# Performance work log

Hardware: AMD Instinct MI355X
Metric: run time of the kernel (lower is better)

## Reference

```python
import jax, jax.numpy as jnp
import numpy as np

N = 20000   # num_perts (nodes)
E = 640000  # edges
H = 2       # attention heads
D = 64      # hidden_dim = out_dim
L = 4       # num_layers
NEG_SLOPE_ATT = 0.2    # GATv2 attention leaky_relu
NEG_SLOPE_ACT = 0.01   # F.leaky_relu default


def setup_inputs() -> dict:
    key = jax.random.key(0)
    ks = jax.random.split(key, 9)
    s = 0.1
    return {
        "edge_index": jax.random.randint(ks[0], (2, E), 0, N, dtype=jnp.int64 if jax.config.x64_enabled else jnp.int32),
        "edge_weight": jax.random.uniform(ks[1], (E,), jnp.float32),
        "pert_emb": jax.random.normal(ks[2], (N, D), jnp.float32) * s,
        "Wl": jax.random.normal(ks[3], (L, D, H * D), jnp.float32) * s,
        "bl": jnp.zeros((L, H * D), jnp.float32),
        "Wr": jax.random.normal(ks[4], (L, D, H * D), jnp.float32) * s,
        "br": jnp.zeros((L, H * D), jnp.float32),
        "att": jax.random.normal(ks[5], (L, H, D), jnp.float32) * s,
        "bias": jnp.zeros((L, D), jnp.float32),
        "Wo": jax.random.normal(ks[6], (D, D), jnp.float32) * s,
        "bo": jnp.zeros((D,), jnp.float32),
    }


def _gatv2_layer(x, src, dst, Wl, bl, Wr, br, att, bias):
    # x: [N, D] -> out: [N, D] (heads averaged, concat=False)
    xl = (x @ Wl + bl).reshape(N, H, D)  # source transform
    xr = (x @ Wr + br).reshape(N, H, D)  # target transform
    e = jax.nn.leaky_relu(xl[src] + xr[dst], NEG_SLOPE_ATT)        # [E,H,D]
    logits = jnp.einsum('ehd,hd->eh', e, att)                      # [E,H]
    # segment softmax over incoming edges per target node
    m = jax.ops.segment_max(logits, dst, num_segments=N)           # [N,H]
    m = jnp.where(jnp.isfinite(m), m, 0.0)
    ex = jnp.exp(logits - m[dst])
    denom = jax.ops.segment_sum(ex, dst, num_segments=N)           # [N,H]
    alpha = ex / (denom[dst] + 1e-16)                              # [E,H]
    msg = xl[src] * alpha[:, :, None]                              # [E,H,D]
    out = jax.ops.segment_sum(msg, dst, num_segments=N)            # [N,H,D]
    return out.mean(axis=1) + bias                                 # [N,D]


def reference(edge_index, edge_weight, pert_emb, Wl, bl, Wr, br, att, bias, Wo, bo):
    del edge_weight  # use_edge_weight=False -> edge_weight set to None
    src, dst = edge_index[0], edge_index[1]
    x = pert_emb  # embedding lookup of arange(num_perts) == full table
    for i in range(L):
        x = _gatv2_layer(x, src, dst, Wl[i], bl[i], Wr[i], br[i], att[i], bias[i])
        x = jax.nn.leaky_relu(x, NEG_SLOPE_ACT)  # dropout p=0.0 is identity
    x = x @ Wo + bo
    x = jax.nn.leaky_relu(x, NEG_SLOPE_ACT)
    return x
```

## Files before the change

### kernel.cpp

```cpp
#include <hip/hip_runtime.h>
#include <hip/hip_fp16.h>
#include <math.h>
#include <float.h>

#define NN 20000
#define EE 640000
#define HH 2
#define DD 64
#define LL 4
#define HD 128
#define CAP 80
#define GR 32
#define GEMM_BLOCKS (NN / GR)
#define SCAT_BLOCKS ((EE + 255) / 256)
#define NPB 4
#define LOG2E 1.4426950408889634f

typedef _Float16 half4 __attribute__((ext_vector_type(4)));
typedef _Float16 half8 __attribute__((ext_vector_type(8)));

__device__ __forceinline__ half4 f2h(float a, float b, float c, float d) {
    half4 r;
    r.x = (_Float16)a; r.y = (_Float16)b; r.z = (_Float16)c; r.w = (_Float16)d;
    return r;
}

__device__ __forceinline__ float grp8_sum(float x) {
    int t;
    t = __builtin_amdgcn_update_dpp(0, __float_as_int(x), 0xB1, 0xF, 0xF, true);
    x += __int_as_float(t);
    t = __builtin_amdgcn_update_dpp(0, __float_as_int(x), 0x4E, 0xF, 0xF, true);
    x += __int_as_float(t);
    t = __builtin_amdgcn_update_dpp(0, __float_as_int(x), 0x141, 0xF, 0xF, true);
    x += __int_as_float(t);
    return x;
}

__global__ void __launch_bounds__(256) prep_kernel(
        const float* __restrict__ x,
        const float* __restrict__ Wl, const float* __restrict__ bl,
        const float* __restrict__ Wr, const float* __restrict__ br,
        _Float16* __restrict__ xl, _Float16* __restrict__ xr,
        const int* __restrict__ src, const int* __restrict__ dst,
        int* __restrict__ cnt, int* __restrict__ csr_src) {
    int tid = threadIdx.x;
    if (blockIdx.x >= GEMM_BLOCKS) {
        int e = (blockIdx.x - GEMM_BLOCKS) * 256 + tid;
        if (e < EE) {
            int d = dst[e];
            int pos = atomicAdd(&cnt[d], 1);
            if (pos < CAP) csr_src[d * CAP + pos] = src[e];
        }
        return;
    }
    __shared__ float xs[16][GR];
    __shared__ float ws[16][2 * HD];
    int row0 = blockIdx.x * GR;
    int tc = tid & 63;
    int tr = tid >> 6;
    int c0 = tc * 4;

    float4 bv;
    {
        const float* bsrc = (c0 < HD) ? (bl + c0) : (br + (c0 - HD));
        bv = *(const float4*)bsrc;
    }
    float acc[8][4];
#pragma unroll
    for (int r = 0; r < 8; ++r) {
        acc[r][0] = bv.x; acc[r][1] = bv.y; acc[r][2] = bv.z; acc[r][3] = bv.w;
    }

    int sr = tid >> 3;
    int skk = (tid & 7) * 2;

    for (int kc = 0; kc < DD; kc += 16) {
        __syncthreads();
        {
            float2 v = *(const float2*)&x[(size_t)(row0 + sr) * DD + kc + skk];
            xs[skk][sr] = v.x;
            xs[skk + 1][sr] = v.y;
        }
#pragma unroll
        for (int q = 0; q < 4; ++q) {
            int idx = tid + 256 * q;
            int kk = idx >> 6;
            int cc = (idx & 63) * 4;
            const float* srcp = (cc < HD) ? (Wl + (size_t)(kc + kk) * HD + cc)
                                          : (Wr + (size_t)(kc + kk) * HD + (cc - HD));
            *(float4*)&ws[kk][cc] = *(const float4*)srcp;
        }
        __syncthreads();
#pragma unroll
        for (int kk = 0; kk < 16; ++kk) {
            float4 wv = *(const float4*)&ws[kk][c0];
            float xv[8];
            *(float4*)&xv[0] = *(const float4*)&xs[kk][tr * 8];
            *(float4*)&xv[4] = *(const float4*)&xs[kk][tr * 8 + 4];
#pragma unroll
            for (int r = 0; r < 8; ++r) {
                acc[r][0] = fmaf(xv[r], wv.x, acc[r][0]);
                acc[r][1] = fmaf(xv[r], wv.y, acc[r][1]);
                acc[r][2] = fmaf(xv[r], wv.z, acc[r][2]);
                acc[r][3] = fmaf(xv[r], wv.w, acc[r][3]);
            }
        }
    }

    _Float16* ybase = (c0 < HD) ? xl : xr;
    int cw = (c0 < HD) ? c0 : (c0 - HD);
#pragma unroll
    for (int r = 0; r < 8; ++r) {
        int row = row0 + tr * 8 + r;
        *(half4*)&ybase[(size_t)row * HD + cw] =
            f2h(acc[r][0], acc[r][1], acc[r][2], acc[r][3]);
    }
}

template <bool FINAL>
__global__ void __launch_bounds__(256, 4) fused_aggregate(
        const _Float16* __restrict__ xl, const _Float16* __restrict__ xr,
        const float* __restrict__ att, const int* __restrict__ cnt,
        const int* __restrict__ csr_src, const float* __restrict__ bias,
        const float* __restrict__ Wnl, const float* __restrict__ bnl,
        const float* __restrict__ Wnr, const float* __restrict__ bnr,
        const float* __restrict__ Wo, const float* __restrict__ bo,
        _Float16* __restrict__ xlo, _Float16* __restrict__ xro,
        float* __restrict__ out) {
    int tid = threadIdx.x;
    int lane = tid & 63;
    int w = tid >> 6;
    int node = blockIdx.x * NPB + w;
    int g = lane >> 4;
    int hl = lane & 15;
    int eo = hl * 8;

    __shared__ float sh_o[NPB][DD];
    __shared__ float wst[16][2 * HD];
    __shared__ int   sh_idx[NPB][CAP];

    int start = node * CAP;
    int deg = min(cnt[node], CAP);

    if (lane < CAP / 2) {
        *(int2*)&sh_idx[w][lane * 2] = *(const int2*)&csr_src[start + lane * 2];
    }
    if (lane >= deg) sh_idx[w][lane] = 0;
    {
        int t2 = lane + 64;
        if (t2 >= deg && t2 < CAP) sh_idx[w][t2] = 0;
    }

    unsigned nrow = (unsigned)node << 7;
    const _Float16* xl_eo = xl + eo;

    float xr0, xr1, xr2, xr3, xr4, xr5, xr6, xr7;
    float at0, at1, at2, at3, at4, at5, at6, at7;
    {
        half8 xh = *(const half8*)&xr[nrow + eo];
        xr0 = (float)xh[0]; xr1 = (float)xh[1]; xr2 = (float)xh[2]; xr3 = (float)xh[3];
        xr4 = (float)xh[4]; xr5 = (float)xh[5]; xr6 = (float)xh[6]; xr7 = (float)xh[7];
        float4 a0 = *(const float4*)&att[eo];
        float4 a1 = *(const float4*)&att[eo + 4];
        at0 = a0.x * LOG2E; at1 = a0.y * LOG2E; at2 = a0.z * LOG2E; at3 = a0.w * LOG2E;
        at4 = a1.x * LOG2E; at5 = a1.y * LOG2E; at6 = a1.z * LOG2E; at7 = a1.w * LOG2E;
    }

    float s = 0.f;
    float ac0 = 0.f, ac1 = 0.f, ac2 = 0.f, ac3 = 0.f;
    float ac4 = 0.f, ac5 = 0.f, ac6 = 0.f, ac7 = 0.f;

    if (deg > 0) {
        int niter = (deg + 7) >> 3;

#define IDX2(k) (*(const int2*)&sh_idx[w][8 * min((k), CAP / 8 - 1) + 2 * g])

#define GATHER(H0, H1, k)                                                  \
        {                                                                  \
            int2 r_ = IDX2(k);                                             \
            H0 = *(const half8*)&xl_eo[(unsigned)r_.x << 7];               \
            H1 = *(const half8*)&xl_eo[(unsigned)r_.y << 7];               \
        }

#define COMPUTE(H0, H1, k)                                                 \
        {                                                                  \
            float x00 = (float)H0[0], x01 = (float)H0[1];                  \
            float x02 = (float)H0[2], x03 = (float)H0[3];                  \
            float x04 = (float)H0[4], x05 = (float)H0[5];                  \
            float x06 = (float)H0[6], x07 = (float)H0[7];                  \
            float x10 = (float)H1[0], x11 = (float)H1[1];                  \
            float x12 = (float)H1[2], x13 = (float)H1[3];                  \
            float x14 = (float)H1[4], x15 = (float)H1[5];                  \
            float x16 = (float)H1[6], x17 = (float)H1[7];                  \
            float v, t0 = 0.f, t1 = 0.f;                                   \
            v = x00 + xr0; v = fmaxf(v, 0.2f * v); t0 = fmaf(v, at0, t0);  \
            v = x01 + xr1; v = fmaxf(v, 0.2f * v); t0 = fmaf(v, at1, t0);  \
            v = x02 + xr2; v = fmaxf(v, 0.2f * v); t0 = fmaf(v, at2, t0);  \
            v = x03 + xr3; v = fmaxf(v, 0.2f * v); t0 = fmaf(v, at3, t0);  \
            v = x04 + xr4; v = fmaxf(v, 0.2f * v); t0 = fmaf(v, at4, t0);  \
            v = x05 + xr5; v = fmaxf(v, 0.2f * v); t0 = fmaf(v, at5, t0);  \
            v = x06 + xr6; v = fmaxf(v, 0.2f * v); t0 = fmaf(v, at6, t0);  \
            v = x07 + xr7; v = fmaxf(v, 0.2f * v); t0 = fmaf(v, at7, t0);  \
            v = x10 + xr0; v = fmaxf(v, 0.2f * v); t1 = fmaf(v, at0, t1);  \
            v = x11 + xr1; v = fmaxf(v, 0.2f * v); t1 = fmaf(v, at1, t1);  \
            v = x12 + xr2; v = fmaxf(v, 0.2f * v); t1 = fmaf(v, at2, t1);  \
            v = x13 + xr3; v = fmaxf(v, 0.2f * v); t1 = fmaf(v, at3, t1);  \
            v = x14 + xr4; v = fmaxf(v, 0.2f * v); t1 = fmaf(v, at4, t1);  \
            v = x15 + xr5; v = fmaxf(v, 0.2f * v); t1 = fmaf(v, at5, t1);  \
            v = x16 + xr6; v = fmaxf(v, 0.2f * v); t1 = fmaf(v, at6, t1);  \
            v = x17 + xr7; v = fmaxf(v, 0.2f * v); t1 = fmaf(v, at7, t1);  \
            t0 = grp8_sum(t0);                                             \
            t1 = grp8_sum(t1);                                             \
            int sl_ = 8 * (k) + 2 * g;                                     \
            float w0 = (sl_ < deg) ? exp2f(t0) : 0.f;                      \
            float w1 = (sl_ + 1 < deg) ? exp2f(t1) : 0.f;                  \
            s += w0 + w1;                                                  \
            ac0 = fmaf(w0, x00, fmaf(w1, x10, ac0));                       \
            ac1 = fmaf(w0, x01, fmaf(w1, x11, ac1));                       \
            ac2 = fmaf(w0, x02, fmaf(w1, x12, ac2));                       \
            ac3 = fmaf(w0, x03, fmaf(w1, x13, ac3));                       \
            ac4 = fmaf(w0, x04, fmaf(w1, x14, ac4));                       \
            ac5 = fmaf(w0, x05, fmaf(w1, x15, ac5));                       \
            ac6 = fmaf(w0, x06, fmaf(w1, x16, ac6));                       \
            ac7 = fmaf(w0, x07, fmaf(w1, x17, ac7));                       \
        }

        half8 A0, A1, B0, B1, C0, C1, D0, D1;

        GATHER(A0, A1, 0);
        GATHER(B0, B1, 1);
        GATHER(C0, C1, 2);

        int it = 0;
        while (true) {
            {
                GATHER(D0, D1, it + 3);
                __builtin_amdgcn_sched_barrier(0);
                COMPUTE(A0, A1, it);
            }
            if (++it == niter) break;
            {
                GATHER(A0, A1, it + 3);
                __builtin_amdgcn_sched_barrier(0);
                COMPUTE(B0, B1, it);
            }
            if (++it == niter) break;
            {
                GATHER(B0, B1, it + 3);
                __builtin_amdgcn_sched_barrier(0);
                COMPUTE(C0, C1, it);
            }
            if (++it == niter) break;
            {
                GATHER(C0, C1, it + 3);
                __builtin_amdgcn_sched_barrier(0);
                COMPUTE(D0, D1, it);
            }
            if (++it == niter) break;
        }
#undef IDX2
#undef GATHER
#undef COMPUTE
    }

#pragma unroll
    for (int off = 16; off <= 32; off <<= 1) {
        s   += __shfl_xor(s, off);
        ac0 += __shfl_xor(ac0, off);
        ac1 += __shfl_xor(ac1, off);
        ac2 += __shfl_xor(ac2, off);
        ac3 += __shfl_xor(ac3, off);
        ac4 += __shfl_xor(ac4, off);
        ac5 += __shfl_xor(ac5, off);
        ac6 += __shfl_xor(ac6, off);
        ac7 += __shfl_xor(ac7, off);
    }

    float so  = __shfl_xor(s, 8);
    float ot0 = __shfl_xor(ac0, 8);
    float ot1 = __shfl_xor(ac1, 8);
    float ot2 = __shfl_xor(ac2, 8);
    float ot3 = __shfl_xor(ac3, 8);
    float ot4 = __shfl_xor(ac4, 8);
    float ot5 = __shfl_xor(ac5, 8);
    float ot6 = __shfl_xor(ac6, 8);
    float ot7 = __shfl_xor(ac7, 8);

    if (lane < 8) {
        float inv0 = 1.0f / (s + 1e-16f);
        float inv1 = 1.0f / (so + 1e-16f);
        float4 bv0 = *(const float4*)&bias[lane * 8];
        float4 bv1 = *(const float4*)&bias[lane * 8 + 4];
        float o0 = fmaf(0.5f, fmaf(ac0, inv0, ot0 * inv1), bv0.x);
        float o1 = fmaf(0.5f, fmaf(ac1, inv0, ot1 * inv1), bv0.y);
        float o2 = fmaf(0.5f, fmaf(ac2, inv0, ot2 * inv1), bv0.z);
        float o3 = fmaf(0.5f, fmaf(ac3, inv0, ot3 * inv1), bv0.w);
        float o4 = fmaf(0.5f, fmaf(ac4, inv0, ot4 * inv1), bv1.x);
        float o5 = fmaf(0.5f, fmaf(ac5, inv0, ot5 * inv1), bv1.y);
        float o6 = fmaf(0.5f, fmaf(ac6, inv0, ot6 * inv1), bv1.z);
        float o7 = fmaf(0.5f, fmaf(ac7, inv0, ot7 * inv1), bv1.w);
        o0 = o0 > 0.f ? o0 : 0.01f * o0;
        o1 = o1 > 0.f ? o1 : 0.01f * o1;
        o2 = o2 > 0.f ? o2 : 0.01f * o2;
        o3 = o3 > 0.f ? o3 : 0.01f * o3;
        o4 = o4 > 0.f ? o4 : 0.01f * o4;
        o5 = o5 > 0.f ? o5 : 0.01f * o5;
        o6 = o6 > 0.f ? o6 : 0.01f * o6;
        o7 = o7 > 0.f ? o7 : 0.01f * o7;
        *(float4*)&sh_o[w][lane * 8]     = make_float4(o0, o1, o2, o3);
        *(float4*)&sh_o[w][lane * 8 + 4] = make_float4(o4, o5, o6, o7);
    }

    if (FINAL) {
        float* wlin = &wst[0][0];
        {
            int idx = tid * 16;
            *(float4*)&wlin[idx]      = *(const float4*)&Wo[idx];
            *(float4*)&wlin[idx + 4]  = *(const float4*)&Wo[idx + 4];
            *(float4*)&wlin[idx + 8]  = *(const float4*)&Wo[idx + 8];
            *(float4*)&wlin[idx + 12] = *(const float4*)&Wo[idx + 12];
        }
        __syncthreads();
        int j = lane;
        float og = bo[j];
#pragma unroll 8
        for (int k = 0; k < DD; ++k) {
            og = fmaf(sh_o[w][k], wlin[k * DD + j], og);
        }
        og = og > 0.f ? og : 0.01f * og;
        out[(size_t)node * DD + j] = og;
    } else {
        int c0 = lane * 4;
        float4 acc4;
        {
            const float* bsrc = (c0 < HD) ? (bnl + c0) : (bnr + (c0 - HD));
            acc4 = *(const float4*)bsrc;
        }
        for (int kc = 0; kc < DD; kc += 16) {
            __syncthreads();
#pragma unroll
            for (int q = 0; q < 4; ++q) {
                int idx = tid + 256 * q;
                int kk = idx >> 6;
                int cc = (idx & 63) * 4;
                const float* p = (cc < HD) ? (Wnl + (size_t)(kc + kk) * HD + cc)
                                           : (Wnr + (size_t)(kc + kk) * HD + (cc - HD));
                *(float4*)&wst[kk][cc] = *(const float4*)p;
            }
            __syncthreads();
#pragma unroll
            for (int kk = 0; kk < 16; ++kk) {
                float xo = sh_o[w][kc + kk];
                float4 wv = *(const float4*)&wst[kk][c0];
                acc4.x = fmaf(xo, wv.x, acc4.x);
                acc4.y = fmaf(xo, wv.y, acc4.y);
                acc4.z = fmaf(xo, wv.z, acc4.z);
                acc4.w = fmaf(xo, wv.w, acc4.w);
            }
        }
        half4 hv = f2h(acc4.x, acc4.y, acc4.z, acc4.w);
        if (c0 < HD) *(half4*)&xlo[(size_t)node * HD + c0] = hv;
        else         *(half4*)&xro[(size_t)node * HD + (c0 - HD)] = hv;
    }
}

extern "C" void kernel_launch(void* const* d_in, const int* in_sizes, int n_in,
                              void* d_out, int out_size, void* d_ws, size_t ws_size,
                              hipStream_t stream) {
    const int* edge_index = (const int*)d_in[0];
    const int* src = edge_index;
    const int* dst = edge_index + EE;
    const float* pert = (const float*)d_in[2];
    const float* Wl = (const float*)d_in[3];
    const float* bl = (const float*)d_in[4];
    const float* Wr = (const float*)d_in[5];
    const float* br = (const float*)d_in[6];
    const float* att = (const float*)d_in[7];
    const float* bias = (const float*)d_in[8];
    const float* Wo = (const float*)d_in[9];
    const float* bo = (const float*)d_in[10];
    float* out = (float*)d_out;

    char* w = (char*)d_ws;
    _Float16* xlA = (_Float16*)w;     w += (size_t)NN * HD * 2;
    _Float16* xrA = (_Float16*)w;     w += (size_t)NN * HD * 2;
    _Float16* xlB = (_Float16*)w;     w += (size_t)NN * HD * 2;
    _Float16* xrB = (_Float16*)w;     w += (size_t)NN * HD * 2;
    int* cnt = (int*)w;               w += (size_t)NN * 4;
    int* csr_src = (int*)w;           w += (size_t)NN * CAP * 4;

    hipMemsetAsync(cnt, 0, (size_t)NN * 4, stream);
    prep_kernel<<<GEMM_BLOCKS + SCAT_BLOCKS, 256, 0, stream>>>(
        pert, Wl, bl, Wr, br, xlA, xrA, src, dst, cnt, csr_src);

    _Float16* xls[2] = {xlA, xlB};
    _Float16* xrs[2] = {xrA, xrB};
    for (int l = 0; l < LL - 1; ++l) {
        fused_aggregate<false><<<NN / NPB, 256, 0, stream>>>(
            xls[l & 1], xrs[l & 1], att + (size_t)l * HD, cnt, csr_src,
            bias + (size_t)l * DD,
            Wl + (size_t)(l + 1) * DD * HD, bl + (size_t)(l + 1) * HD,
            Wr + (size_t)(l + 1) * DD * HD, br + (size_t)(l + 1) * HD,
            nullptr, nullptr,
            xls[(l + 1) & 1], xrs[(l + 1) & 1], nullptr);
    }
    fused_aggregate<true><<<NN / NPB, 256, 0, stream>>>(
        xls[(LL - 1) & 1], xrs[(LL - 1) & 1], att + (size_t)(LL - 1) * HD, cnt, csr_src,
        bias + (size_t)(LL - 1) * DD,
        nullptr, nullptr, nullptr, nullptr,
        Wo, bo, nullptr, nullptr, out);
}
```

Baseline: 270.0 us.

## Precompute fp16 transposed next-layer weights and use fdot2 for fused projection

Adds extra prep blocks that convert the next-layer Wl/Wr to fp16, transposed column-major with an 8-element k grouping. The aggregate kernel then loads the whole 256x64 fp16 weight into padded LDS in one go, replacing four float tiles and their barrier pairs. It computes the projection with packed fp16 dot-product instructions. This cuts LDS traffic, barriers and FMA count in the per-node GEMV, at the cost of fp16 activations and weights in the projection, plus a larger LDS footprint (about 36KB) that may lower occupancy.

After: 261.2 us (median of 2 runs). 3.3% less time.

```diff
diff --git a/kernel.cpp b/kernel.cpp
--- a/kernel.cpp
+++ b/kernel.cpp
@@ -13,11 +13,21 @@
 #define GR 32
 #define GEMM_BLOCKS (NN / GR)
 #define SCAT_BLOCKS ((EE + 255) / 256)
+#define WCVT_BLOCKS 24
 #define NPB 4
 #define LOG2E 1.4426950408889634f
-
+#define PADK 72
+
+typedef _Float16 hh2 __attribute__((ext_vector_type(2)));
 typedef _Float16 half4 __attribute__((ext_vector_type(4)));
 typedef _Float16 half8 __attribute__((ext_vector_type(8)));
+
+#if __has_builtin(__builtin_amdgcn_fdot2)
+#define FDOT2(a, b, c) __builtin_amdgcn_fdot2((a), (b), (c), false)
+#else
+#define FDOT2(a, b, c) fmaf((float)(a)[0], (float)(b)[0], \
+                        fmaf((float)(a)[1], (float)(b)[1], (c)))
+#endif
 
 __device__ __forceinline__ half4 f2h(float a, float b, float c, float d) {
     half4 r;
@@ -42,8 +52,31 @@
         const float* __restrict__ Wr, const float* __restrict__ br,
         _Float16* __restrict__ xl, _Float16* __restrict__ xr,
         const int* __restrict__ src, const int* __restrict__ dst,
-        int* __restrict__ cnt, int* __restrict__ csr_src) {
+        int* __restrict__ cnt, int* __restrict__ csr_src,
+        _Float16* __restrict__ wt16) {
     int tid = threadIdx.x;
+    if (blockIdx.x >= GEMM_BLOCKS + SCAT_BLOCKS) {
+        int q = (blockIdx.x - GEMM_BLOCKS - SCAT_BLOCKS) * 256 + tid;
+        int l = q >> 11;
+        int r = q & 2047;
+        int col = r >> 3;
+        int kb = r & 7;
+        const float* base = (col < HD)
+            ? (Wl + (size_t)(l + 1) * DD * HD + col)
+            : (Wr + (size_t)(l + 1) * DD * HD + (col - HD));
+        base += (size_t)(kb * 8) * HD;
+        half8 h;
+        h[0] = (_Float16)base[0 * HD];
+        h[1] = (_Float16)base[1 * HD];
+        h[2] = (_Float16)base[2 * HD];
+        h[3] = (_Float16)base[3 * HD];
+        h[4] = (_Float16)base[4 * HD];
+        h[5] = (_Float16)base[5 * HD];
+        h[6] = (_Float16)base[6 * HD];
+        h[7] = (_Float16)base[7 * HD];
+        *(half8*)&wt16[(size_t)l * 16384 + (size_t)r * 8] = h;
+        return;
+    }
     if (blockIdx.x >= GEMM_BLOCKS) {
         int e = (blockIdx.x - GEMM_BLOCKS) * 256 + tid;
         if (e < EE) {
@@ -122,8 +155,8 @@
         const _Float16* __restrict__ xl, const _Float16* __restrict__ xr,
         const float* __restrict__ att, const int* __restrict__ cnt,
         const int* __restrict__ csr_src, const float* __restrict__ bias,
-        const float* __restrict__ Wnl, const float* __restrict__ bnl,
-        const float* __restrict__ Wnr, const float* __restrict__ bnr,
+        const _Float16* __restrict__ wtn, const float* __restrict__ bnl,
+        const float* __restrict__ bnr,
         const float* __restrict__ Wo, const float* __restrict__ bo,
         _Float16* __restrict__ xlo, _Float16* __restrict__ xro,
         float* __restrict__ out) {
@@ -135,9 +168,9 @@
     int hl = lane & 15;
     int eo = hl * 8;
 
-    __shared__ float sh_o[NPB][DD];
-    __shared__ float wst[16][2 * HD];
-    __shared__ int   sh_idx[NPB][CAP];
+    __shared__ float    sh_o[NPB][DD];
+    __shared__ _Float16 sh_o16[NPB][DD];
+    __shared__ int      sh_idx[NPB][CAP];
 
     int start = node * CAP;
     int deg = min(cnt[node], CAP);
@@ -263,6 +296,9 @@
 #undef COMPUTE
     }
 
+    asm volatile("" ::: "memory");
+    __builtin_amdgcn_sched_barrier(0);
+
 #pragma unroll
     for (int off = 16; off <= 32; off <<= 1) {
         s   += __shfl_xor(s, off);
@@ -307,12 +343,21 @@
         o5 = o5 > 0.f ? o5 : 0.01f * o5;
         o6 = o6 > 0.f ? o6 : 0.01f * o6;
         o7 = o7 > 0.f ? o7 : 0.01f * o7;
-        *(float4*)&sh_o[w][lane * 8]     = make_float4(o0, o1, o2, o3);
-        *(float4*)&sh_o[w][lane * 8 + 4] = make_float4(o4, o5, o6, o7);
+        if (FINAL) {
+            *(float4*)&sh_o[w][lane * 8]     = make_float4(o0, o1, o2, o3);
+            *(float4*)&sh_o[w][lane * 8 + 4] = make_float4(o4, o5, o6, o7);
+        } else {
+            half8 h;
+            h[0] = (_Float16)o0; h[1] = (_Float16)o1;
+            h[2] = (_Float16)o2; h[3] = (_Float16)o3;
+            h[4] = (_Float16)o4; h[5] = (_Float16)o5;
+            h[6] = (_Float16)o6; h[7] = (_Float16)o7;
+            *(half8*)&sh_o16[w][lane * 8] = h;
+        }
     }
 
     if (FINAL) {
-        float* wlin = &wst[0][0];
+        __shared__ float wlin[DD * DD];
         {
             int idx = tid * 16;
             *(float4*)&wlin[idx]      = *(const float4*)&Wo[idx];
@@ -330,37 +375,63 @@
         og = og > 0.f ? og : 0.01f * og;
         out[(size_t)node * DD + j] = og;
     } else {
-        int c0 = lane * 4;
-        float4 acc4;
-        {
-            const float* bsrc = (c0 < HD) ? (bnl + c0) : (bnr + (c0 - HD));
-            acc4 = *(const float4*)bsrc;
-        }
-        for (int kc = 0; kc < DD; kc += 16) {
-            __syncthreads();
-#pragma unroll
-            for (int q = 0; q < 4; ++q) {
-                int idx = tid + 256 * q;
-                int kk = idx >> 6;
-                int cc = (idx & 63) * 4;
-                const float* p = (cc < HD) ? (Wnl + (size_t)(kc + kk) * HD + cc)
-                                           : (Wnr + (size_t)(kc + kk) * HD + (cc - HD));
-                *(float4*)&wst[kk][cc] = *(const float4*)p;
-            }
-            __syncthreads();
-#pragma unroll
-            for (int kk = 0; kk < 16; ++kk) {
-                float xo = sh_o[w][kc + kk];
-                float4 wv = *(const float4*)&wst[kk][c0];
-                acc4.x = fmaf(xo, wv.x, acc4.x);
-                acc4.y = fmaf(xo, wv.y, acc4.y);
-                acc4.z = fmaf(xo, wv.z, acc4.z);
-                acc4.w = fmaf(xo, wv.w, acc4.w);
-            }
-        }
-        half4 hv = f2h(acc4.x, acc4.y, acc4.z, acc4.w);
-        if (c0 < HD) *(half4*)&xlo[(size_t)node * HD + c0] = hv;
-        else         *(half4*)&xro[(size_t)node * HD + (c0 - HD)] = hv;
+        __shared__ _Float16 wt[256 * PADK];
+#pragma unroll
+        for (int i = 0; i < 8; ++i) {
+            int q = tid + 256 * i;
+            int col = q >> 3;
+            int kb = q & 7;
+            half8 hv = *(const half8*)&wtn[(size_t)q * 8];
+            *(half8*)&wt[col * PADK + kb * 8] = hv;
+        }
+        __syncthreads();
+
+        float a0 = bnl[lane];
+        float a1 = bnl[lane + 64];
+        float a2 = bnr[lane];
+        float a3 = bnr[lane + 64];
+        const _Float16* o16p = &sh_o16[w][0];
+        const _Float16* w0p = &wt[(lane)       * PADK];
+        const _Float16* w1p = &wt[(lane + 64)  * PADK];
+        const _Float16* w2p = &wt[(lane + 128) * PADK];
+        const _Float16* w3p = &wt[(lane + 192) * PADK];
+
+#define KB(kb)                                                             \
+        {                                                                  \
+            half8 o8 = *(const half8*)&o16p[(kb) * 8];                     \
+            half8 wa = *(const half8*)&w0p[(kb) * 8];                      \
+            half8 wb = *(const half8*)&w1p[(kb) * 8];                      \
+            half8 wc = *(const half8*)&w2p[(kb) * 8];                      \
+            half8 wd = *(const half8*)&w3p[(kb) * 8];                      \
+            hh2 oA = __builtin_shufflevector(o8, o8, 0, 1);                \
+            hh2 oB = __builtin_shufflevector(o8, o8, 2, 3);                \
+            hh2 oC = __builtin_shufflevector(o8, o8, 4, 5);                \
+            hh2 oD = __builtin_shufflevector(o8, o8, 6, 7);                \
+            a0 = FDOT2(__builtin_shufflevector(wa, wa, 0, 1), oA, a0);     \
+            a0 = FDOT2(__builtin_shufflevector(wa, wa, 2, 3), oB, a0);     \
+            a0 = FDOT2(__builtin_shufflevector(wa, wa, 4, 5), oC, a0);     \
+            a0 = FDOT2(__builtin_shufflevector(wa, wa, 6, 7), oD, a0);     \
+            a1 = FDOT2(__builtin_shufflevector(wb, wb, 0, 1), oA, a1);     \
+            a1 = FDOT2(__builtin_shufflevector(wb, wb, 2, 3), oB, a1);     \
+            a1 = FDOT2(__builtin_shufflevector(wb, wb, 4, 5), oC, a1);     \
+            a1 = FDOT2(__builtin_shufflevector(wb, wb, 6, 7), oD, a1);     \
+            a2 = FDOT2(__builtin_shufflevector(wc, wc, 0, 1), oA, a2);     \
+            a2 = FDOT2(__builtin_shufflevector(wc, wc, 2, 3), oB, a2);     \
+            a2 = FDOT2(__builtin_shufflevector(wc, wc, 4, 5), oC, a2);     \
+            a2 = FDOT2(__builtin_shufflevector(wc, wc, 6, 7), oD, a2);     \
+            a3 = FDOT2(__builtin_shufflevector(wd, wd, 0, 1), oA, a3);     \
+            a3 = FDOT2(__builtin_shufflevector(wd, wd, 2, 3), oB, a3);     \
+            a3 = FDOT2(__builtin_shufflevector(wd, wd, 4, 5), oC, a3);     \
+            a3 = FDOT2(__builtin_shufflevector(wd, wd, 6, 7), oD, a3);     \
+        }
+        KB(0) KB(1) KB(2) KB(3) KB(4) KB(5) KB(6) KB(7)
+#undef KB
+
+        size_t nb = (size_t)node * HD;
+        xlo[nb + lane]      = (_Float16)a0;
+        xlo[nb + lane + 64] = (_Float16)a1;
+        xro[nb + lane]      = (_Float16)a2;
+        xro[nb + lane + 64] = (_Float16)a3;
     }
 }
 
@@ -388,10 +459,11 @@
     _Float16* xrB = (_Float16*)w;     w += (size_t)NN * HD * 2;
     int* cnt = (int*)w;               w += (size_t)NN * 4;
     int* csr_src = (int*)w;           w += (size_t)NN * CAP * 4;
+    _Float16* wt16 = (_Float16*)w;    w += (size_t)3 * 256 * DD * 2;
 
     hipMemsetAsync(cnt, 0, (size_t)NN * 4, stream);
-    prep_kernel<<<GEMM_BLOCKS + SCAT_BLOCKS, 256, 0, stream>>>(
-        pert, Wl, bl, Wr, br, xlA, xrA, src, dst, cnt, csr_src);
+    prep_kernel<<<GEMM_BLOCKS + SCAT_BLOCKS + WCVT_BLOCKS, 256, 0, stream>>>(
+        pert, Wl, bl, Wr, br, xlA, xrA, src, dst, cnt, csr_src, wt16);
 
     _Float16* xls[2] = {xlA, xlB};
     _Float16* xrs[2] = {xrA, xrB};
@@ -399,14 +471,14 @@
         fused_aggregate<false><<<NN / NPB, 256, 0, stream>>>(
             xls[l & 1], xrs[l & 1], att + (size_t)l * HD, cnt, csr_src,
             bias + (size_t)l * DD,
-            Wl + (size_t)(l + 1) * DD * HD, bl + (size_t)(l + 1) * HD,
-            Wr + (size_t)(l + 1) * DD * HD, br + (size_t)(l + 1) * HD,
+            wt16 + (size_t)l * 16384,
+            bl + (size_t)(l + 1) * HD, br + (size_t)(l + 1) * HD,
             nullptr, nullptr,
             xls[(l + 1) & 1], xrs[(l + 1) & 1], nullptr);
     }
     fused_aggregate<true><<<NN / NPB, 256, 0, stream>>>(
         xls[(LL - 1) & 1], xrs[(LL - 1) & 1], att + (size_t)(LL - 1) * HD, cnt, csr_src,
         bias + (size_t)(LL - 1) * DD,
-        nullptr, nullptr, nullptr, nullptr,
+        nullptr, nullptr, nullptr,
         Wo, bo, nullptr, nullptr, out);
 }
```
